# Performance work log

Hardware: AMD Instinct MI355X
Metric: run time of the kernel (lower is better)

## Reference

```python
import jax, jax.numpy as jnp
import numpy as np

E, H, S, NH, B = 32768, 256, 32, 8, 64
HD = H // NH


def setup_inputs() -> dict:
    key = jax.random.key(0)
    ks = jax.random.split(key, 13)
    sc = 1.0 / np.sqrt(H)
    return {
        "edge_features": jax.random.normal(ks[0], (E, H), jnp.float32),
        "edge_coords": jax.random.normal(ks[1], (E, 3), jnp.float32),
        "batch": jnp.sort(jax.random.randint(ks[2], (E,), 0, B, dtype=jnp.int32)),
        "seed_vectors": jax.random.normal(ks[3], (S, H), jnp.float32),
        "Wq": jax.random.normal(ks[4], (H, H), jnp.float32) * sc,
        "Wk": jax.random.normal(ks[5], (H, H), jnp.float32) * sc,
        "Wv": jax.random.normal(ks[6], (H, H), jnp.float32) * sc,
        "Wo": jax.random.normal(ks[7], (H, H), jnp.float32) * sc,
        "bo": jnp.zeros((H,), jnp.float32),
        "W1": jax.random.normal(ks[8], (H, S * H), jnp.float32) / np.sqrt(S * H),
        "b1": jnp.zeros((H,), jnp.float32),
        "W2": jax.random.normal(ks[9], (H, H), jnp.float32) * sc,
        "b2": jnp.zeros((H,), jnp.float32),
    }


def reference(edge_features, edge_coords, batch, seed_vectors,
              Wq, Wk, Wv, Wo, bo, W1, b1, W2, b2):
    # Per-graph PMA cross-attention: shared seed queries attend over each
    # graph's ragged set of edges (segment softmax), then out_proj + MLP.
    # edge_coords is unused by the original forward.
    q = (seed_vectors @ Wq.T).reshape(S, NH, HD)          # [S, nh, hd]
    k = (edge_features @ Wk.T).reshape(E, NH, HD)         # [E, nh, hd]
    v = (edge_features @ Wv.T).reshape(E, NH, HD)         # [E, nh, hd]

    scores = jnp.einsum('shd,ehd->ehs', q, k) / (HD ** 0.5)   # [E, nh, S]
    # segment (per-graph) stable softmax over the edge axis
    smax = jax.ops.segment_max(scores, batch, num_segments=B,
                               indices_are_sorted=True)        # [B, nh, S]
    ex = jnp.exp(scores - smax[batch])
    denom = jax.ops.segment_sum(ex, batch, num_segments=B,
                                indices_are_sorted=True)       # [B, nh, S]
    w = ex / denom[batch]                                      # [E, nh, S]

    # attended[b, nh, S, hd] = sum_{e in graph b} w[e,nh,S] * v[e,nh,hd]
    attended = jax.ops.segment_sum(w[:, :, :, None] * v[:, :, None, :],
                                   batch, num_segments=B,
                                   indices_are_sorted=True)    # [B, nh, S, hd]
    attended = attended.transpose(0, 2, 1, 3).reshape(B, S, H)  # [B, S, H]

    graph_repr = attended @ Wo.T + bo                           # [B, S, H]
    flat = graph_repr.reshape(B, S * H)
    h1 = jax.nn.silu(flat @ W1.T + b1)                          # [B, H]
    return h1 @ W2.T + b2                                       # [B, H]
```

## Files before the change

### kernel.cpp

```cpp
#include <hip/hip_runtime.h>
#include <hip/hip_bf16.h>

#define E_N 32768
#define H_N 256
#define S_N 32
#define NH_N 8
#define B_N 64

typedef _Float16 f16x8 __attribute__((ext_vector_type(8)));
typedef _Float16 f16x4 __attribute__((ext_vector_type(4)));
typedef float    f32x4 __attribute__((ext_vector_type(4)));

#define OFF_MTH    0
#define OFF_MP     65536
#define OFF_SP     196608
#define OFF_MM     327680
#define OFF_DI     344064
#define OFF_ATT    360448
#define OFF_GR     884736
#define OFF_PART   1409024
#define OFF_H1     2457600
#define OFF_SCORES 2473984
#define OFF_VH     10862592

__device__ inline int lower_bound64(const int* __restrict__ batch, int b) {
    int lo = 0, hi = E_N;
    while (lo < hi) { int mid = (lo + hi) >> 1; if (batch[mid] < b) lo = mid + 1; else hi = mid; }
    return lo;
}

__global__ __launch_bounds__(256) void prep(const float* __restrict__ seed,
                                            const float* __restrict__ Wq,
                                            const float* __restrict__ Wk,
                                            const float* __restrict__ Wv,
                                            _Float16* __restrict__ Mth) {
    const int t = threadIdx.x, bid = blockIdx.x;
    if (bid < 8) {
        const int nh = bid;
        __shared__ float q_l[32][32];
        const int d = t & 31, s0 = t >> 5;
        float a0 = 0, a1 = 0, a2 = 0, a3 = 0;
        const float* wq = &Wq[(nh * 32 + d) * 256];
        for (int j = 0; j < 256; ++j) {
            float w = wq[j];
            a0 += w * seed[(s0) * 256 + j];
            a1 += w * seed[(s0 + 8) * 256 + j];
            a2 += w * seed[(s0 + 16) * 256 + j];
            a3 += w * seed[(s0 + 24) * 256 + j];
        }
        q_l[s0][d] = a0; q_l[s0 + 8][d] = a1; q_l[s0 + 16][d] = a2; q_l[s0 + 24][d] = a3;
        __syncthreads();
        float acc[32];
#pragma unroll
        for (int s = 0; s < 32; ++s) acc[s] = 0.f;
        for (int dd = 0; dd < 32; ++dd) {
            float w = Wk[(nh * 32 + dd) * 256 + t];
#pragma unroll
            for (int s = 0; s < 32; ++s) acc[s] += w * q_l[s][dd];
        }
        const float scale = 0.17677669529663687f;
        for (int s = 0; s < 32; ++s)
            Mth[(nh * 32 + s) * 256 + t] = (_Float16)(acc[s] * scale);
    } else {
        const int j0 = (bid - 8) * 32;
        for (int jj = 0; jj < 32; ++jj)
            Mth[(256 + j0 + jj) * 256 + t] = (_Float16)Wv[(j0 + jj) * 256 + t];
    }
}

__global__ __launch_bounds__(256) void gemm16(const float* __restrict__ X,
                                              const _Float16* __restrict__ Mth,
                                              float* __restrict__ scores,
                                              _Float16* __restrict__ vh) {
    __shared__ _Float16 As[128][72];
    __shared__ _Float16 Bs[128][72];
    const int tid = threadIdx.x;
    const int n0 = blockIdx.x * 128;
    const int m0 = blockIdx.y * 128;
    const int w = tid >> 6, l = tid & 63;
    const int lr = l & 15, kg = l >> 4;
    const int wr = (w & 1) * 64, wc = (w >> 1) * 64;
    f32x4 acc[4][4] = {};

    for (int ks = 0; ks < 4; ++ks) {
        const int k0 = ks * 64;
#pragma unroll
        for (int i = 0; i < 8; ++i) {
            int idx = tid + i * 256;
            int row = idx >> 4, c4 = (idx & 15) * 4;
            float4 xv = *(const float4*)&X[(m0 + row) * 256 + k0 + c4];
            f16x4 h;
            h[0] = (_Float16)xv.x; h[1] = (_Float16)xv.y;
            h[2] = (_Float16)xv.z; h[3] = (_Float16)xv.w;
            *(f16x4*)&As[row][c4] = h;
        }
#pragma unroll
        for (int i = 0; i < 4; ++i) {
            int idx = tid + i * 256;
            int row = idx >> 3, c8 = (idx & 7) * 8;
            *(uint4*)&Bs[row][c8] = *(const uint4*)&Mth[(n0 + row) * 256 + k0 + c8];
        }
        __syncthreads();
#pragma unroll
        for (int kk = 0; kk < 2; ++kk) {
            f16x8 af[4], bf[4];
#pragma unroll
            for (int mr = 0; mr < 4; ++mr)
                af[mr] = *(const f16x8*)&As[wr + mr * 16 + lr][kk * 32 + kg * 8];
#pragma unroll
            for (int nc = 0; nc < 4; ++nc)
                bf[nc] = *(const f16x8*)&Bs[wc + nc * 16 + lr][kk * 32 + kg * 8];
#pragma unroll
            for (int mr = 0; mr < 4; ++mr)
#pragma unroll
                for (int nc = 0; nc < 4; ++nc)
                    acc[mr][nc] = __builtin_amdgcn_mfma_f32_16x16x32_f16(
                        af[mr], bf[nc], acc[mr][nc], 0, 0, 0);
        }
        __syncthreads();
    }
    const int r0 = m0 + wr + kg * 4;
    if (n0 < 256) {
#pragma unroll
        for (int mr = 0; mr < 4; ++mr)
#pragma unroll
            for (int nc = 0; nc < 4; ++nc) {
                int col = n0 + wc + nc * 16 + lr;
#pragma unroll
                for (int j = 0; j < 4; ++j)
                    scores[(r0 + mr * 16 + j) * 256 + col] = acc[mr][nc][j];
            }
    } else {
#pragma unroll
        for (int mr = 0; mr < 4; ++mr)
#pragma unroll
            for (int nc = 0; nc < 4; ++nc) {
                int col = n0 - 256 + wc + nc * 16 + lr;
#pragma unroll
                for (int j = 0; j < 4; ++j)
                    vh[(r0 + mr * 16 + j) * 256 + col] = (_Float16)acc[mr][nc][j];
            }
    }
}

__global__ __launch_bounds__(256) void stats_partial(const float* __restrict__ scores,
                                                     const int* __restrict__ batch,
                                                     float* __restrict__ mp,
                                                     float* __restrict__ sp) {
    const int b = blockIdx.x, c = blockIdx.y, t = threadIdx.x;
    const int e0 = lower_bound64(batch, b);
    const int e1 = lower_bound64(batch, b + 1);
    const int len = e1 - e0;
    const int cs = e0 + (len * c) / 8;
    const int ce = e0 + (len * (c + 1)) / 8;
    float m = -3.4e38f;
    for (int e = cs; e < ce; ++e) m = fmaxf(m, scores[e * 256 + t]);
    float s = 0.f;
    for (int e = cs; e < ce; ++e) s += __expf(scores[e * 256 + t] - m);
    mp[(b * 8 + c) * 256 + t] = m;
    sp[(b * 8 + c) * 256 + t] = s;
}

__global__ __launch_bounds__(256) void stats_merge(const float* __restrict__ mp,
                                                   const float* __restrict__ sp,
                                                   float* __restrict__ mm,
                                                   float* __restrict__ di) {
    const int b = blockIdx.x, t = threadIdx.x;
    float m = -3.4e38f;
#pragma unroll
    for (int c = 0; c < 8; ++c) m = fmaxf(m, mp[(b * 8 + c) * 256 + t]);
    float d = 0.f;
#pragma unroll
    for (int c = 0; c < 8; ++c) {
        float sc = sp[(b * 8 + c) * 256 + t];
        if (sc > 0.f) d += sc * __expf(mp[(b * 8 + c) * 256 + t] - m);
    }
    mm[b * 256 + t] = m;
    di[b * 256 + t] = (d > 0.f) ? 1.f / d : 0.f;
}

__global__ __launch_bounds__(256) void attend(const float* __restrict__ scores,
                                              const _Float16* __restrict__ vh,
                                              const int* __restrict__ batch,
                                              const float* __restrict__ mm,
                                              const float* __restrict__ di,
                                              float* __restrict__ att) {
    const int b = blockIdx.x, nh = blockIdx.y, t = threadIdx.x;
    const int e0 = lower_bound64(batch, b);
    const int e1 = lower_bound64(batch, b + 1);
    __shared__ float wl[32][33];
    __shared__ float vl[32][33];
    __shared__ float mc[32], dc[32];
    if (t < 32) {
        mc[t] = mm[b * 256 + nh * 32 + t];
        dc[t] = di[b * 256 + nh * 32 + t];
    }
    __syncthreads();
    const int s = t & 31, g = t >> 5;
    const int le = t >> 3, q = t & 7;
    float acc0 = 0.f, acc1 = 0.f, acc2 = 0.f, acc3 = 0.f;
    for (int te = e0; te < e1; te += 32) {
        const int e = te + le;
        const bool ok = (e < e1);
        float4 x = make_float4(0.f, 0.f, 0.f, 0.f);
        f16x4 vv = {};
        if (ok) {
            x = *(const float4*)&scores[e * 256 + nh * 32 + q * 4];
            vv = *(const f16x4*)&vh[e * 256 + nh * 32 + q * 4];
        }
        wl[le][q * 4 + 0] = ok ? __expf(x.x - mc[q * 4 + 0]) : 0.f;
        wl[le][q * 4 + 1] = ok ? __expf(x.y - mc[q * 4 + 1]) : 0.f;
        wl[le][q * 4 + 2] = ok ? __expf(x.z - mc[q * 4 + 2]) : 0.f;
        wl[le][q * 4 + 3] = ok ? __expf(x.w - mc[q * 4 + 3]) : 0.f;
        vl[le][q * 4 + 0] = ok ? (float)vv[0] : 0.f;
        vl[le][q * 4 + 1] = ok ? (float)vv[1] : 0.f;
        vl[le][q * 4 + 2] = ok ? (float)vv[2] : 0.f;
        vl[le][q * 4 + 3] = ok ? (float)vv[3] : 0.f;
        __syncthreads();
#pragma unroll
        for (int e2 = 0; e2 < 32; ++e2) {
            float wv = wl[e2][s];
            acc0 += wv * vl[e2][g * 4 + 0];
            acc1 += wv * vl[e2][g * 4 + 1];
            acc2 += wv * vl[e2][g * 4 + 2];
            acc3 += wv * vl[e2][g * 4 + 3];
        }
        __syncthreads();
    }
    const float dv = dc[s];
    float* op = &att[(b * 32 + s) * 256 + nh * 32 + g * 4];
    op[0] = acc0 * dv; op[1] = acc1 * dv; op[2] = acc2 * dv; op[3] = acc3 * dv;
}

__global__ __launch_bounds__(256) void gemm_abT(const float* __restrict__ A,
                                                const float* __restrict__ W,
                                                const float* __restrict__ bias,
                                                float* __restrict__ out0) {
    __shared__ float As[16][64];
    __shared__ float Bs[16][64];
    const int tid = threadIdx.x;
    const int m0 = blockIdx.y * 64, n0 = blockIdx.x * 64;
    const int tx = tid & 15, ty = tid >> 4;
    const int lrow = tid >> 2;
    const int lkq = (tid & 3) * 4;
    float acc[4][4];
#pragma unroll
    for (int i = 0; i < 4; ++i)
#pragma unroll
        for (int j = 0; j < 4; ++j) acc[i][j] = 0.f;

    for (int k0 = 0; k0 < 256; k0 += 16) {
        float4 av = *(const float4*)&A[(m0 + lrow) * 256 + k0 + lkq];
        float4 wv = *(const float4*)&W[(n0 + lrow) * 256 + k0 + lkq];
        As[lkq + 0][lrow] = av.x; As[lkq + 1][lrow] = av.y;
        As[lkq + 2][lrow] = av.z; As[lkq + 3][lrow] = av.w;
        Bs[lkq + 0][lrow] = wv.x; Bs[lkq + 1][lrow] = wv.y;
        Bs[lkq + 2][lrow] = wv.z; Bs[lkq + 3][lrow] = wv.w;
        __syncthreads();
#pragma unroll
        for (int k = 0; k < 16; ++k) {
            float4 a4 = *(const float4*)&As[k][ty * 4];
            float4 b4 = *(const float4*)&Bs[k][tx * 4];
            acc[0][0] += a4.x * b4.x; acc[0][1] += a4.x * b4.y;
            acc[0][2] += a4.x * b4.z; acc[0][3] += a4.x * b4.w;
            acc[1][0] += a4.y * b4.x; acc[1][1] += a4.y * b4.y;
            acc[1][2] += a4.y * b4.z; acc[1][3] += a4.y * b4.w;
            acc[2][0] += a4.z * b4.x; acc[2][1] += a4.z * b4.y;
            acc[2][2] += a4.z * b4.z; acc[2][3] += a4.z * b4.w;
            acc[3][0] += a4.w * b4.x; acc[3][1] += a4.w * b4.y;
            acc[3][2] += a4.w * b4.z; acc[3][3] += a4.w * b4.w;
        }
        __syncthreads();
    }
    const int c = n0 + tx * 4;
    float4 bb = bias ? *(const float4*)&bias[c]
                     : make_float4(0.f, 0.f, 0.f, 0.f);
#pragma unroll
    for (int mi = 0; mi < 4; ++mi) {
        int r = m0 + ty * 4 + mi;
        float4 o = make_float4(acc[mi][0] + bb.x, acc[mi][1] + bb.y,
                               acc[mi][2] + bb.z, acc[mi][3] + bb.w);
        *(float4*)&out0[r * 256 + c] = o;
    }
}

__global__ __launch_bounds__(256) void gemm_w1_splitk(const float* __restrict__ flat,
                                                      const float* __restrict__ W1,
                                                      float* __restrict__ partials) {
    __shared__ float As[16][64];
    __shared__ float Bs[16][64];
    const int tid = threadIdx.x;
    const int n0 = blockIdx.x * 64;
    const int kbase = blockIdx.y * 128;
    const int tx = tid & 15, ty = tid >> 4;
    const int lrow = tid >> 2, lkq = (tid & 3) * 4;
    float acc[4][4];
#pragma unroll
    for (int i = 0; i < 4; ++i)
#pragma unroll
        for (int j = 0; j < 4; ++j) acc[i][j] = 0.f;

    for (int k0 = 0; k0 < 128; k0 += 16) {
        float4 av = *(const float4*)&flat[lrow * 8192 + kbase + k0 + lkq];
        float4 wv = *(const float4*)&W1[(n0 + lrow) * 8192 + kbase + k0 + lkq];
        As[lkq + 0][lrow] = av.x; As[lkq + 1][lrow] = av.y;
        As[lkq + 2][lrow] = av.z; As[lkq + 3][lrow] = av.w;
        Bs[lkq + 0][lrow] = wv.x; Bs[lkq + 1][lrow] = wv.y;
        Bs[lkq + 2][lrow] = wv.z; Bs[lkq + 3][lrow] = wv.w;
        __syncthreads();
#pragma unroll
        for (int k = 0; k < 16; ++k) {
            float4 a4 = *(const float4*)&As[k][ty * 4];
            float4 b4 = *(const float4*)&Bs[k][tx * 4];
            acc[0][0] += a4.x * b4.x; acc[0][1] += a4.x * b4.y;
            acc[0][2] += a4.x * b4.z; acc[0][3] += a4.x * b4.w;
            acc[1][0] += a4.y * b4.x; acc[1][1] += a4.y * b4.y;
            acc[1][2] += a4.y * b4.z; acc[1][3] += a4.y * b4.w;
            acc[2][0] += a4.z * b4.x; acc[2][1] += a4.z * b4.y;
            acc[2][2] += a4.z * b4.z; acc[2][3] += a4.z * b4.w;
            acc[3][0] += a4.w * b4.x; acc[3][1] += a4.w * b4.y;
            acc[3][2] += a4.w * b4.z; acc[3][3] += a4.w * b4.w;
        }
        __syncthreads();
    }
#pragma unroll
    for (int mi = 0; mi < 4; ++mi) {
        int bb = ty * 4 + mi;
        *(float4*)&partials[blockIdx.y * 16384 + bb * 256 + n0 + tx * 4] =
            make_float4(acc[mi][0], acc[mi][1], acc[mi][2], acc[mi][3]);
    }
}

__global__ void silu_reduce(const float* __restrict__ partials,
                            const float* __restrict__ b1,
                            float* __restrict__ h1) {
    int t = blockIdx.x * 256 + threadIdx.x;
    float sum = b1[t & 255];
    for (int ks = 0; ks < 64; ++ks) sum += partials[ks * 16384 + t];
    h1[t] = sum / (1.f + __expf(-sum));
}

extern "C" void kernel_launch(void* const* d_in, const int* in_sizes, int n_in,
                              void* d_out, int out_size, void* d_ws, size_t ws_size,
                              hipStream_t stream) {
    const float* X     = (const float*)d_in[0];
    const int*   batch = (const int*)d_in[2];
    const float* seed  = (const float*)d_in[3];
    const float* Wq    = (const float*)d_in[4];
    const float* Wk    = (const float*)d_in[5];
    const float* Wv    = (const float*)d_in[6];
    const float* Wo    = (const float*)d_in[7];
    const float* bo    = (const float*)d_in[8];
    const float* W1    = (const float*)d_in[9];
    const float* b1    = (const float*)d_in[10];
    const float* W2    = (const float*)d_in[11];
    const float* b2    = (const float*)d_in[12];
    float* out = (float*)d_out;
    float* ws = (float*)d_ws;

    _Float16* Mth   = (_Float16*)(ws + OFF_MTH);
    float* mp       = ws + OFF_MP;
    float* sp       = ws + OFF_SP;
    float* mm       = ws + OFF_MM;
    float* di       = ws + OFF_DI;
    float* att      = ws + OFF_ATT;
    float* gr       = ws + OFF_GR;
    float* part     = ws + OFF_PART;
    float* h1       = ws + OFF_H1;
    float* scores   = ws + OFF_SCORES;
    _Float16* vh    = (_Float16*)(ws + OFF_VH);

    hipLaunchKernelGGL(prep, dim3(16), dim3(256), 0, stream, seed, Wq, Wk, Wv, Mth);
    hipLaunchKernelGGL(gemm16, dim3(4, 256), dim3(256), 0, stream, X, Mth, scores, vh);
    hipLaunchKernelGGL(stats_partial, dim3(64, 8), dim3(256), 0, stream, scores, batch, mp, sp);
    hipLaunchKernelGGL(stats_merge, dim3(64), dim3(256), 0, stream, mp, sp, mm, di);
    hipLaunchKernelGGL(attend, dim3(64, 8), dim3(256), 0, stream, scores, vh, batch, mm, di, att);
    hipLaunchKernelGGL(gemm_abT, dim3(4, 32), dim3(256), 0, stream, att, Wo, bo, gr);
    hipLaunchKernelGGL(gemm_w1_splitk, dim3(4, 64), dim3(256), 0, stream, gr, W1, part);
    hipLaunchKernelGGL(silu_reduce, dim3(64), dim3(256), 0, stream, part, b1, h1);
    hipLaunchKernelGGL(gemm_abT, dim3(4, 1), dim3(256), 0, stream, h1, W2, b2, out);
}
```

Measured before the change: 273.9 us.

## Split segment softmax stats and attention over more edge chunks with reduction

Stats partials now split each graph into 32 edge chunks instead of 8, with 4-way unrolled independent max/sum accumulators. The attend kernel adds a z-dimension that splits each graph's edges into 4 chunks writing separate partial outputs, summed by a new attend_reduce kernel. The silu reduction is also unrolled with multiple accumulators. The aim is more blocks in flight to fill the GPU and more memory-level parallelism, at the cost of extra workspace traffic and one more launch.

```diff
diff --git a/kernel.cpp b/kernel.cpp
--- a/kernel.cpp
+++ b/kernel.cpp
@@ -12,16 +12,17 @@
 typedef float    f32x4 __attribute__((ext_vector_type(4)));
 
 #define OFF_MTH    0
-#define OFF_MP     65536
-#define OFF_SP     196608
-#define OFF_MM     327680
-#define OFF_DI     344064
-#define OFF_ATT    360448
-#define OFF_GR     884736
-#define OFF_PART   1409024
-#define OFF_H1     2457600
-#define OFF_SCORES 2473984
-#define OFF_VH     10862592
+#define OFF_MM     65536
+#define OFF_DI     81920
+#define OFF_MP     98304
+#define OFF_SP     622592
+#define OFF_ATT4   98304
+#define OFF_ATT    2195456
+#define OFF_GR     2719744
+#define OFF_PART   3244032
+#define OFF_H1     4292608
+#define OFF_SCORES 4308992
+#define OFF_VH     12697600
 
 __device__ inline int lower_bound64(const int* __restrict__ batch, int b) {
     int lo = 0, hi = E_N;
@@ -151,14 +152,29 @@
     const int e0 = lower_bound64(batch, b);
     const int e1 = lower_bound64(batch, b + 1);
     const int len = e1 - e0;
-    const int cs = e0 + (len * c) / 8;
-    const int ce = e0 + (len * (c + 1)) / 8;
-    float m = -3.4e38f;
-    for (int e = cs; e < ce; ++e) m = fmaxf(m, scores[e * 256 + t]);
-    float s = 0.f;
-    for (int e = cs; e < ce; ++e) s += __expf(scores[e * 256 + t] - m);
-    mp[(b * 8 + c) * 256 + t] = m;
-    sp[(b * 8 + c) * 256 + t] = s;
+    const int cs = e0 + (len * c) / 32;
+    const int ce = e0 + (len * (c + 1)) / 32;
+    float m0 = -3.4e38f, m1 = -3.4e38f, m2 = -3.4e38f, m3 = -3.4e38f;
+    int e = cs;
+    for (; e + 4 <= ce; e += 4) {
+        m0 = fmaxf(m0, scores[(e + 0) * 256 + t]);
+        m1 = fmaxf(m1, scores[(e + 1) * 256 + t]);
+        m2 = fmaxf(m2, scores[(e + 2) * 256 + t]);
+        m3 = fmaxf(m3, scores[(e + 3) * 256 + t]);
+    }
+    for (; e < ce; ++e) m0 = fmaxf(m0, scores[e * 256 + t]);
+    float m = fmaxf(fmaxf(m0, m1), fmaxf(m2, m3));
+    float s0 = 0.f, s1 = 0.f, s2 = 0.f, s3 = 0.f;
+    e = cs;
+    for (; e + 4 <= ce; e += 4) {
+        s0 += __expf(scores[(e + 0) * 256 + t] - m);
+        s1 += __expf(scores[(e + 1) * 256 + t] - m);
+        s2 += __expf(scores[(e + 2) * 256 + t] - m);
+        s3 += __expf(scores[(e + 3) * 256 + t] - m);
+    }
+    for (; e < ce; ++e) s0 += __expf(scores[e * 256 + t] - m);
+    mp[(b * 32 + c) * 256 + t] = m;
+    sp[(b * 32 + c) * 256 + t] = (s0 + s1) + (s2 + s3);
 }
 
 __global__ __launch_bounds__(256) void stats_merge(const float* __restrict__ mp,
@@ -168,12 +184,12 @@
     const int b = blockIdx.x, t = threadIdx.x;
     float m = -3.4e38f;
 #pragma unroll
-    for (int c = 0; c < 8; ++c) m = fmaxf(m, mp[(b * 8 + c) * 256 + t]);
+    for (int c = 0; c < 32; ++c) m = fmaxf(m, mp[(b * 32 + c) * 256 + t]);
     float d = 0.f;
 #pragma unroll
-    for (int c = 0; c < 8; ++c) {
-        float sc = sp[(b * 8 + c) * 256 + t];
-        if (sc > 0.f) d += sc * __expf(mp[(b * 8 + c) * 256 + t] - m);
+    for (int c = 0; c < 32; ++c) {
+        float sc = sp[(b * 32 + c) * 256 + t];
+        if (sc > 0.f) d += sc * __expf(mp[(b * 32 + c) * 256 + t] - m);
     }
     mm[b * 256 + t] = m;
     di[b * 256 + t] = (d > 0.f) ? 1.f / d : 0.f;
@@ -184,10 +200,13 @@
                                               const int* __restrict__ batch,
                                               const float* __restrict__ mm,
                                               const float* __restrict__ di,
-                                              float* __restrict__ att) {
-    const int b = blockIdx.x, nh = blockIdx.y, t = threadIdx.x;
+                                              float* __restrict__ att4) {
+    const int b = blockIdx.x, nh = blockIdx.y, c = blockIdx.z, t = threadIdx.x;
     const int e0 = lower_bound64(batch, b);
     const int e1 = lower_bound64(batch, b + 1);
+    const int len = e1 - e0;
+    const int cs = e0 + (len * c) / 4;
+    const int ce = e0 + (len * (c + 1)) / 4;
     __shared__ float wl[32][33];
     __shared__ float vl[32][33];
     __shared__ float mc[32], dc[32];
@@ -199,9 +218,9 @@
     const int s = t & 31, g = t >> 5;
     const int le = t >> 3, q = t & 7;
     float acc0 = 0.f, acc1 = 0.f, acc2 = 0.f, acc3 = 0.f;
-    for (int te = e0; te < e1; te += 32) {
+    for (int te = cs; te < ce; te += 32) {
         const int e = te + le;
-        const bool ok = (e < e1);
+        const bool ok = (e < ce);
         float4 x = make_float4(0.f, 0.f, 0.f, 0.f);
         f16x4 vv = {};
         if (ok) {
@@ -228,8 +247,19 @@
         __syncthreads();
     }
     const float dv = dc[s];
-    float* op = &att[(b * 32 + s) * 256 + nh * 32 + g * 4];
+    float* op = &att4[((size_t)c * 2048 + b * 32 + s) * 256 + nh * 32 + g * 4];
     op[0] = acc0 * dv; op[1] = acc1 * dv; op[2] = acc2 * dv; op[3] = acc3 * dv;
+}
+
+__global__ __launch_bounds__(256) void attend_reduce(const float* __restrict__ att4,
+                                                     float* __restrict__ att) {
+    const int i = (blockIdx.x * 256 + threadIdx.x) * 4;
+    float4 a = *(const float4*)&att4[i];
+    float4 b = *(const float4*)&att4[524288 + i];
+    float4 c = *(const float4*)&att4[2 * 524288 + i];
+    float4 d = *(const float4*)&att4[3 * 524288 + i];
+    *(float4*)&att[i] = make_float4(a.x + b.x + c.x + d.x, a.y + b.y + c.y + d.y,
+                                    a.z + b.z + c.z + d.z, a.w + b.w + c.w + d.w);
 }
 
 __global__ __launch_bounds__(256) void gemm_abT(const float* __restrict__ A,
@@ -335,8 +365,15 @@
                             const float* __restrict__ b1,
                             float* __restrict__ h1) {
     int t = blockIdx.x * 256 + threadIdx.x;
-    float sum = b1[t & 255];
-    for (int ks = 0; ks < 64; ++ks) sum += partials[ks * 16384 + t];
+    float s0 = b1[t & 255], s1 = 0.f, s2 = 0.f, s3 = 0.f;
+#pragma unroll
+    for (int ks = 0; ks < 64; ks += 4) {
+        s0 += partials[(ks + 0) * 16384 + t];
+        s1 += partials[(ks + 1) * 16384 + t];
+        s2 += partials[(ks + 2) * 16384 + t];
+        s3 += partials[(ks + 3) * 16384 + t];
+    }
+    float sum = (s0 + s1) + (s2 + s3);
     h1[t] = sum / (1.f + __expf(-sum));
 }
 
@@ -359,10 +396,11 @@
     float* ws = (float*)d_ws;
 
     _Float16* Mth   = (_Float16*)(ws + OFF_MTH);
+    float* mm       = ws + OFF_MM;
+    float* di       = ws + OFF_DI;
     float* mp       = ws + OFF_MP;
     float* sp       = ws + OFF_SP;
-    float* mm       = ws + OFF_MM;
-    float* di       = ws + OFF_DI;
+    float* att4     = ws + OFF_ATT4;
     float* att      = ws + OFF_ATT;
     float* gr       = ws + OFF_GR;
     float* part     = ws + OFF_PART;
@@ -372,9 +410,10 @@
 
     hipLaunchKernelGGL(prep, dim3(16), dim3(256), 0, stream, seed, Wq, Wk, Wv, Mth);
     hipLaunchKernelGGL(gemm16, dim3(4, 256), dim3(256), 0, stream, X, Mth, scores, vh);
-    hipLaunchKernelGGL(stats_partial, dim3(64, 8), dim3(256), 0, stream, scores, batch, mp, sp);
+    hipLaunchKernelGGL(stats_partial, dim3(64, 32), dim3(256), 0, stream, scores, batch, mp, sp);
     hipLaunchKernelGGL(stats_merge, dim3(64), dim3(256), 0, stream, mp, sp, mm, di);
-    hipLaunchKernelGGL(attend, dim3(64, 8), dim3(256), 0, stream, scores, vh, batch, mm, di, att);
+    hipLaunchKernelGGL(attend, dim3(64, 8, 4), dim3(256), 0, stream, scores, vh, batch, mm, di, att4);
+    hipLaunchKernelGGL(attend_reduce, dim3(512), dim3(256), 0, stream, att4, att);
     hipLaunchKernelGGL(gemm_abT, dim3(4, 32), dim3(256), 0, stream, att, Wo, bo, gr);
     hipLaunchKernelGGL(gemm_w1_splitk, dim3(4, 64), dim3(256), 0, stream, gr, W1, part);
     hipLaunchKernelGGL(silu_reduce, dim3(64), dim3(256), 0, stream, part, b1, h1);
```

Measured after the change: 247.5 us. 1.11x faster.
